# Optimization experiments

Hardware: AMD Instinct MI355X
Metric: run time of the kernel (lower is better)

## Reference

```python
import jax, jax.numpy as jnp
import numpy as np

R = 48          # n_comp (== n_comp_xy)
X = Y = Z = 300 # world_size
C = 27          # channels
N = 1_000_000   # query points
XYZ_MIN = 0.0
XYZ_MAX = 1.0


def _sample2d(plane, gh, gw):
    """Bilinear grid_sample, align_corners=True.
    plane: [R, H, W]; gh, gw: [N] normalized coords in [-1, 1] indexing H and W.
    Returns [N, R].
    """
    H, W = plane.shape[1], plane.shape[2]
    ih = (gh + 1.0) * 0.5 * (H - 1)
    iw = (gw + 1.0) * 0.5 * (W - 1)
    i0 = jnp.clip(jnp.floor(ih).astype(jnp.int32), 0, H - 1)
    j0 = jnp.clip(jnp.floor(iw).astype(jnp.int32), 0, W - 1)
    i1 = jnp.minimum(i0 + 1, H - 1)
    j1 = jnp.minimum(j0 + 1, W - 1)
    fh = (ih - i0.astype(ih.dtype))[:, None]  # [N,1]
    fw = (iw - j0.astype(iw.dtype))[:, None]
    p00 = plane[:, i0, j0].T  # [N,R]
    p01 = plane[:, i0, j1].T
    p10 = plane[:, i1, j0].T
    p11 = plane[:, i1, j1].T
    top = p00 * (1 - fw) + p01 * fw
    bot = p10 * (1 - fw) + p11 * fw
    return top * (1 - fh) + bot * fh


def _sample1d(vec, g):
    """Linear interp along length dim (width of the [*,*,L,1] torch vec is 1,
    sampled at 0 -> pure 1D interp).  vec: [R, L]; g: [N] in [-1,1] -> [N,R]."""
    L = vec.shape[1]
    ih = (g + 1.0) * 0.5 * (L - 1)
    i0 = jnp.clip(jnp.floor(ih).astype(jnp.int32), 0, L - 1)
    i1 = jnp.minimum(i0 + 1, L - 1)
    f = (ih - i0.astype(ih.dtype))[:, None]
    return vec[:, i0].T * (1 - f) + vec[:, i1].T * f


def setup_inputs() -> dict:
    key = jax.random.key(0)
    ks = jax.random.split(key, 8)
    return {
        "xyz": jax.random.uniform(ks[0], (N, 3), dtype=jnp.float32),
        "xy_plane": jax.random.normal(ks[1], (R, X, Y), dtype=jnp.float32) * 0.1,
        "xz_plane": jax.random.normal(ks[2], (R, X, Z), dtype=jnp.float32) * 0.1,
        "yz_plane": jax.random.normal(ks[3], (R, Y, Z), dtype=jnp.float32) * 0.1,
        "x_vec": jax.random.normal(ks[4], (R, X), dtype=jnp.float32) * 0.1,
        "y_vec": jax.random.normal(ks[5], (R, Y), dtype=jnp.float32) * 0.1,
        "z_vec": jax.random.normal(ks[6], (R, Z), dtype=jnp.float32) * 0.1,
        "f_vec": jax.random.uniform(ks[7], (3 * R, C), dtype=jnp.float32,
                                     minval=-0.1, maxval=0.1),
    }


def reference(xyz, xy_plane, xz_plane, yz_plane, x_vec, y_vec, z_vec, f_vec):
    # normalize to [-1, 1]
    g = (xyz - XYZ_MIN) / (XYZ_MAX - XYZ_MIN) * 2.0 - 1.0  # [N,3]
    gx, gy, gz = g[:, 0], g[:, 1], g[:, 2]
    xy_feat = _sample2d(xy_plane, gx, gy)  # [N,R]
    xz_feat = _sample2d(xz_plane, gx, gz)
    yz_feat = _sample2d(yz_plane, gy, gz)
    x_feat = _sample1d(x_vec, gx)
    y_feat = _sample1d(y_vec, gy)
    z_feat = _sample1d(z_vec, gz)
    feat = jnp.concatenate([xy_feat * z_feat, xz_feat * y_feat, yz_feat * x_feat],
                           axis=-1)  # [N, 3R]
    return feat @ f_vec  # [N, C]
```

## Files before the change

### kernel.cpp

```cpp
#include <hip/hip_runtime.h>

#define RR 48
#define GG 300
#define HW2 (GG * GG)
#define NPLANE (RR * HW2)
#define NVEC (RR * GG)
#define CC 27
#define NBUCK 32768
#define TP 64
#define TPP 65

struct Axis { int i0, i1; float f; };

__device__ __forceinline__ Axis axis_interp(float x) {
  float g = x * 2.0f - 1.0f;
  float ih = (g + 1.0f) * 0.5f * (float)(GG - 1);
  int i0 = (int)floorf(ih);
  i0 = i0 < 0 ? 0 : (i0 > GG - 1 ? GG - 1 : i0);
  int i1 = i0 + 1 > GG - 1 ? GG - 1 : i0 + 1;
  Axis a; a.i0 = i0; a.i1 = i1; a.f = ih - (float)i0;
  return a;
}

__device__ __forceinline__ unsigned part3(unsigned v) {
  unsigned r = 0;
  r |= (v & 1u);
  r |= (v & 2u) << 2;
  r |= (v & 4u) << 4;
  r |= (v & 8u) << 6;
  r |= (v & 16u) << 8;
  return r;
}

__device__ __forceinline__ int morton_key(float x, float y, float z) {
  int qx = (int)(x * 32.0f); qx = qx < 0 ? 0 : (qx > 31 ? 31 : qx);
  int qy = (int)(y * 32.0f); qy = qy < 0 ? 0 : (qy > 31 ? 31 : qy);
  int qz = (int)(z * 32.0f); qz = qz < 0 ? 0 : (qz > 31 ? 31 : qz);
  return (int)(part3((unsigned)qx) | (part3((unsigned)qy) << 1) | (part3((unsigned)qz) << 2));
}

__global__ void __launch_bounds__(256) hist_kernel(const float* __restrict__ xyz, int n,
                                                   int* __restrict__ offs) {
  int i = blockIdx.x * blockDim.x + threadIdx.x;
  if (i >= n) return;
  atomicAdd(&offs[morton_key(xyz[i * 3], xyz[i * 3 + 1], xyz[i * 3 + 2])], 1);
}

__global__ void __launch_bounds__(1024) scan_kernel(int* __restrict__ offs) {
  __shared__ int part[1024];
  int t = threadIdx.x;
  int base = t * (NBUCK / 1024);
  int loc[NBUCK / 1024];
  int s = 0;
#pragma unroll
  for (int i = 0; i < NBUCK / 1024; ++i) { loc[i] = offs[base + i]; s += loc[i]; }
  part[t] = s;
  __syncthreads();
  for (int off = 1; off < 1024; off <<= 1) {
    int u = (t >= off) ? part[t - off] : 0;
    __syncthreads();
    part[t] += u;
    __syncthreads();
  }
  int excl = (t == 0) ? 0 : part[t - 1];
#pragma unroll
  for (int i = 0; i < NBUCK / 1024; ++i) {
    int c = loc[i];
    offs[base + i] = excl;
    excl += c;
  }
}

__global__ void __launch_bounds__(256) scatter_kernel(const float* __restrict__ xyz, int n,
                                                      int* __restrict__ offs,
                                                      int* __restrict__ sidx,
                                                      float4* __restrict__ sxyz) {
  int i = blockIdx.x * blockDim.x + threadIdx.x;
  if (i >= n) return;
  float x = xyz[i * 3], y = xyz[i * 3 + 1], z = xyz[i * 3 + 2];
  int key = morton_key(x, y, z);
  int pos = atomicAdd(&offs[key], 1);
  if (sxyz) {
    sxyz[pos] = make_float4(x, y, z, __int_as_float(i));
  } else {
    sidx[pos] = i;
  }
}

__global__ void __launch_bounds__(256) transpose_planes(const float* __restrict__ p0,
                                                        const float* __restrict__ p1,
                                                        const float* __restrict__ p2,
                                                        float* __restrict__ t0,
                                                        float* __restrict__ t1,
                                                        float* __restrict__ t2) {
  __shared__ float tile[256 * 49];
  const float* in = (blockIdx.y == 0) ? p0 : (blockIdx.y == 1) ? p1 : p2;
  float* out = (blockIdx.y == 0) ? t0 : (blockIdx.y == 1) ? t1 : t2;
  int base = blockIdx.x * 256;
  int t = threadIdx.x;
  int pos = base + t;
#pragma unroll 1
  for (int r = 0; r < RR; ++r) {
    float v = (pos < HW2) ? in[r * HW2 + pos] : 0.f;
    tile[t * 49 + r] = v;
  }
  __syncthreads();
#pragma unroll 1
  for (int k = t; k < 256 * RR; k += 256) {
    int p = k / RR;
    int r = k - p * RR;
    int hw = base + p;
    if (hw < HW2) out[hw * RR + r] = tile[p * 49 + r];
  }
}

__global__ void __launch_bounds__(256) transpose_vecs(const float* __restrict__ v0,
                                                      const float* __restrict__ v1,
                                                      const float* __restrict__ v2,
                                                      float* __restrict__ t0,
                                                      float* __restrict__ t1,
                                                      float* __restrict__ t2) {
  int e = blockIdx.x * blockDim.x + threadIdx.x;
  if (e >= 3 * NVEC) return;
  int v = e / NVEC;
  int rem = e - v * NVEC;
  int i = rem / RR;
  int r = rem - i * RR;
  const float* in = (v == 0) ? v0 : (v == 1) ? v1 : v2;
  float* out = (v == 0) ? t0 : (v == 1) ? t1 : t2;
  out[i * RR + r] = in[r * GG + i];
}

__device__ __forceinline__ void gather_seg(const float* __restrict__ P, Axis ai, Axis aj,
                                           const float* __restrict__ V, Axis ak,
                                           int r4, float* __restrict__ dst) {
  float fi = ai.f, fj = aj.f, fk = ak.f;
  float w00 = (1.f - fi) * (1.f - fj);
  float w01 = (1.f - fi) * fj;
  float w10 = fi * (1.f - fj);
  float w11 = fi * fj;
  float omk = 1.f - fk;
  float4 q00 = *(const float4*)(P + (ai.i0 * GG + aj.i0) * RR + r4);
  float4 q01 = *(const float4*)(P + (ai.i0 * GG + aj.i1) * RR + r4);
  float4 q10 = *(const float4*)(P + (ai.i1 * GG + aj.i0) * RR + r4);
  float4 q11 = *(const float4*)(P + (ai.i1 * GG + aj.i1) * RR + r4);
  float4 b0 = *(const float4*)(V + ak.i0 * RR + r4);
  float4 b1 = *(const float4*)(V + ak.i1 * RR + r4);
  float t0 = (w00 * q00.x + w01 * q01.x + w10 * q10.x + w11 * q11.x) * (omk * b0.x + fk * b1.x);
  float t1 = (w00 * q00.y + w01 * q01.y + w10 * q10.y + w11 * q11.y) * (omk * b0.y + fk * b1.y);
  float t2 = (w00 * q00.z + w01 * q01.z + w10 * q10.z + w11 * q11.z) * (omk * b0.z + fk * b1.z);
  float t3 = (w00 * q00.w + w01 * q01.w + w10 * q10.w + w11 * q11.w) * (omk * b0.w + fk * b1.w);
  dst[(r4 + 0) * TPP] = t0;
  dst[(r4 + 1) * TPP] = t1;
  dst[(r4 + 2) * TPP] = t2;
  dst[(r4 + 3) * TPP] = t3;
}

__global__ void __launch_bounds__(256, 4) tensorf_fused(
    const float4* __restrict__ sxyz, const int* __restrict__ sidx,
    const float* __restrict__ xyz,
    const float* __restrict__ Txy, const float* __restrict__ Txz, const float* __restrict__ Tyz,
    const float* __restrict__ Tx, const float* __restrict__ Ty, const float* __restrict__ Tz,
    const float* __restrict__ F, float* __restrict__ out, int n, int chunkLen) {
  __shared__ float featT[144 * TPP];
  __shared__ int oiS[TP];
  int b = blockIdx.x;
  int nb = (b & 7) * chunkLen + (b >> 3);
  int base = nb * TP;
  int tid = threadIdx.x;
  int g = tid >> 4;
  int l = tid & 15;

#pragma unroll 1
  for (int it = 0; it < TP / 16; ++it) {
    int pl = (it << 4) + g;
    int sp = base + pl;
    if (sp < n) {
      float x, y, z;
      int oi;
      if (sxyz) {
        float4 p4 = sxyz[sp];
        x = p4.x; y = p4.y; z = p4.z;
        oi = __float_as_int(p4.w);
      } else {
        oi = sidx[sp];
        x = xyz[oi * 3 + 0];
        y = xyz[oi * 3 + 1];
        z = xyz[oi * 3 + 2];
      }
      if (l == 12) oiS[pl] = oi;
      Axis ax = axis_interp(x), ay = axis_interp(y), az = axis_interp(z);
      if (l < 12) {
        int r4 = l << 2;
        float* dst = &featT[pl];
        gather_seg(Txy, ax, ay, Tz, az, r4, dst + 0 * RR * TPP);
        gather_seg(Txz, ax, az, Ty, ay, r4, dst + 1 * RR * TPP);
        gather_seg(Tyz, ay, az, Tx, ax, r4, dst + 2 * RR * TPP);
      }
    }
  }
  __syncthreads();

  int p = tid & (TP - 1);
  int q = __builtin_amdgcn_readfirstlane(tid >> 6);
  int cbase = (q == 3) ? 20 : q * 7;
  const float* Fh = F + cbase;

  float acc[7];
#pragma unroll
  for (int c = 0; c < 7; ++c) acc[c] = 0.f;

#pragma unroll 4
  for (int k = 0; k < 144; ++k) {
    float fv = featT[k * TPP + p];
#pragma unroll
    for (int c = 0; c < 7; ++c) acc[c] = fmaf(fv, Fh[k * CC + c], acc[c]);
  }

  int sp = base + p;
  if (sp < n) {
    int oi = oiS[p];
    float* o = out + (size_t)oi * CC + cbase;
    if (q != 3) o[0] = acc[0];
#pragma unroll
    for (int c = 1; c < 7; ++c) o[c] = acc[c];
  }
}

__global__ void __launch_bounds__(256) tensorf_naive(
    const float* __restrict__ xyz,
    const float* __restrict__ Pxy, const float* __restrict__ Pxz, const float* __restrict__ Pyz,
    const float* __restrict__ Vx, const float* __restrict__ Vy, const float* __restrict__ Vz,
    const float* __restrict__ F, float* __restrict__ out, int n) {
  int idx = blockIdx.x * blockDim.x + threadIdx.x;
  if (idx >= n) return;
  float x = xyz[idx * 3], y = xyz[idx * 3 + 1], z = xyz[idx * 3 + 2];
  Axis ax = axis_interp(x), ay = axis_interp(y), az = axis_interp(z);
  float acc[CC];
#pragma unroll
  for (int c = 0; c < CC; ++c) acc[c] = 0.f;
  const float* Ps[3] = {Pxy, Pxz, Pyz};
  const float* Vs[3] = {Vz, Vy, Vx};
  Axis A[3][2] = {{ax, ay}, {ax, az}, {ay, az}};
  Axis K[3] = {az, ay, ax};
#pragma unroll 1
  for (int s = 0; s < 3; ++s) {
    Axis ai = A[s][0], aj = A[s][1], ak = K[s];
    float fi = ai.f, fj = aj.f, fk = ak.f;
    float w00 = (1.f - fi) * (1.f - fj), w01 = (1.f - fi) * fj;
    float w10 = fi * (1.f - fj), w11 = fi * fj, omk = 1.f - fk;
#pragma unroll 1
    for (int r = 0; r < RR; ++r) {
      const float* pr = Ps[s] + r * HW2;
      float ft = (w00 * pr[ai.i0 * GG + aj.i0] + w01 * pr[ai.i0 * GG + aj.i1] +
                  w10 * pr[ai.i1 * GG + aj.i0] + w11 * pr[ai.i1 * GG + aj.i1]) *
                 (omk * Vs[s][r * GG + ak.i0] + fk * Vs[s][r * GG + ak.i1]);
      const float* Fr = F + (s * RR + r) * CC;
#pragma unroll
      for (int c = 0; c < CC; ++c) acc[c] = fmaf(ft, Fr[c], acc[c]);
    }
  }
  float* o = out + (size_t)idx * CC;
#pragma unroll
  for (int c = 0; c < CC; ++c) o[c] = acc[c];
}

extern "C" void kernel_launch(void* const* d_in, const int* in_sizes, int n_in,
                              void* d_out, int out_size, void* d_ws, size_t ws_size,
                              hipStream_t stream) {
  const float* xyz = (const float*)d_in[0];
  const float* pxy = (const float*)d_in[1];
  const float* pxz = (const float*)d_in[2];
  const float* pyz = (const float*)d_in[3];
  const float* vx = (const float*)d_in[4];
  const float* vy = (const float*)d_in[5];
  const float* vz = (const float*)d_in[6];
  const float* F = (const float*)d_in[7];
  float* out = (float*)d_out;
  int n = in_sizes[0] / 3;
  int nblk = (n + 255) / 256;

  size_t fixed = (size_t)(3 * NPLANE + 3 * NVEC) * sizeof(float) +
                 (size_t)NBUCK * sizeof(int);
  size_t need1 = fixed + (size_t)n * sizeof(int);
  size_t need2 = fixed + (size_t)n * sizeof(float4);

  if (ws_size >= need1) {
    float* w = (float*)d_ws;
    float* Txy = w;
    float* Txz = Txy + NPLANE;
    float* Tyz = Txz + NPLANE;
    float* Tx = Tyz + NPLANE;
    float* Ty = Tx + NVEC;
    float* Tz = Ty + NVEC;
    int* offs = (int*)(Tz + NVEC);

    int* sidx = nullptr;
    float4* sxyz = nullptr;
    if (ws_size >= need2) sxyz = (float4*)(offs + NBUCK);
    else sidx = (int*)(offs + NBUCK);

    int tb = (HW2 + 255) / 256;
    dim3 tg(tb, 3);
    transpose_planes<<<tg, 256, 0, stream>>>(pxy, pxz, pyz, Txy, Txz, Tyz);
    int vb = (3 * NVEC + 255) / 256;
    transpose_vecs<<<vb, 256, 0, stream>>>(vx, vy, vz, Tx, Ty, Tz);

    hipMemsetAsync(offs, 0, (size_t)NBUCK * sizeof(int), stream);
    hist_kernel<<<nblk, 256, 0, stream>>>(xyz, n, offs);
    scan_kernel<<<1, 1024, 0, stream>>>(offs);
    scatter_kernel<<<nblk, 256, 0, stream>>>(xyz, n, offs, sidx, sxyz);

    int ntile = (n + TP - 1) / TP;
    int chunkLen = (ntile + 7) / 8;
    tensorf_fused<<<chunkLen * 8, 256, 0, stream>>>(sxyz, sidx, xyz, Txy, Txz, Tyz,
                                                    Tx, Ty, Tz, F, out, n, chunkLen);
  } else {
    tensorf_naive<<<nblk, 256, 0, stream>>>(xyz, pxy, pxz, pyz, vx, vy, vz, F, out, n);
  }
}
```

Before: 598.9 us.

## Fuse plane/vector transposes and histogram into one preprocess kernel with vectorized transpose

Merges the plane transpose, vector transpose and Morton histogram into a single launch, with block index ranges deciding which job each block does. This removes two kernel launches and lets the independent stages overlap. The plane transpose is reworked to use float4 global loads and stores through a row-major shared tile padded to 260 floats, in place of scalar strided accesses. The tile grows to about 50KB of shared memory, which may reduce occupancy for the histogram blocks that share the kernel.

```diff
diff --git a/kernel.cpp b/kernel.cpp
--- a/kernel.cpp
+++ b/kernel.cpp
@@ -10,6 +10,11 @@
 #define TP 64
 #define TPP 65
 
+#define PBLK ((HW2 + 255) / 256)
+#define PB3 (3 * PBLK)
+#define VBLK ((3 * NVEC + 255) / 256)
+#define TROW 260
+
 struct Axis { int i0, i1; float f; };
 
 __device__ __forceinline__ Axis axis_interp(float x) {
@@ -39,11 +44,76 @@
   return (int)(part3((unsigned)qx) | (part3((unsigned)qy) << 1) | (part3((unsigned)qz) << 2));
 }
 
-__global__ void __launch_bounds__(256) hist_kernel(const float* __restrict__ xyz, int n,
-                                                   int* __restrict__ offs) {
-  int i = blockIdx.x * blockDim.x + threadIdx.x;
-  if (i >= n) return;
-  atomicAdd(&offs[morton_key(xyz[i * 3], xyz[i * 3 + 1], xyz[i * 3 + 2])], 1);
+__global__ void __launch_bounds__(256) preprocess_kernel(
+    const float* __restrict__ p0, const float* __restrict__ p1, const float* __restrict__ p2,
+    float* __restrict__ t0, float* __restrict__ t1, float* __restrict__ t2,
+    const float* __restrict__ v0, const float* __restrict__ v1, const float* __restrict__ v2,
+    float* __restrict__ tv0, float* __restrict__ tv1, float* __restrict__ tv2,
+    const float* __restrict__ xyz, int n, int* __restrict__ offs) {
+  __shared__ float tile[RR * TROW];
+  int bb = blockIdx.x;
+  int t = threadIdx.x;
+
+  if (bb < PB3) {
+    int plane = bb / PBLK;
+    int chunk = bb - plane * PBLK;
+    const float* in = (plane == 0) ? p0 : (plane == 1) ? p1 : p2;
+    float* outp = (plane == 0) ? t0 : (plane == 1) ? t1 : t2;
+    int base = chunk * 256;
+    if (base + 256 <= HW2) {
+      int p4 = t & 63;
+      int rg = t >> 6;
+#pragma unroll 1
+      for (int i = 0; i < 12; ++i) {
+        int r = i * 4 + rg;
+        float4 v = *(const float4*)(in + (size_t)r * HW2 + base + p4 * 4);
+        *(float4*)&tile[r * TROW + p4 * 4] = v;
+      }
+      __syncthreads();
+#pragma unroll 1
+      for (int jj = 0; jj < 12; ++jj) {
+        int hw = ((jj & 3) << 6) + (t >> 2);
+        int c4 = ((jj >> 2) << 2) + (t & 3);
+        float4 w;
+        w.x = tile[(c4 * 4 + 0) * TROW + hw];
+        w.y = tile[(c4 * 4 + 1) * TROW + hw];
+        w.z = tile[(c4 * 4 + 2) * TROW + hw];
+        w.w = tile[(c4 * 4 + 3) * TROW + hw];
+        *(float4*)(outp + (size_t)(base + hw) * RR + c4 * 4) = w;
+      }
+    } else {
+      int pos = base + t;
+#pragma unroll 1
+      for (int r = 0; r < RR; ++r) {
+        float v = (pos < HW2) ? in[(size_t)r * HW2 + pos] : 0.f;
+        tile[r * TROW + t] = v;
+      }
+      __syncthreads();
+#pragma unroll 1
+      for (int k = t; k < 256 * RR; k += 256) {
+        int p = k / RR;
+        int r = k - p * RR;
+        int hw = base + p;
+        if (hw < HW2) outp[(size_t)hw * RR + r] = tile[r * TROW + p];
+      }
+    }
+  } else if (bb < PB3 + VBLK) {
+    int e = (bb - PB3) * 256 + t;
+    if (e < 3 * NVEC) {
+      int v = e / NVEC;
+      int rem = e - v * NVEC;
+      int i = rem / RR;
+      int r = rem - i * RR;
+      const float* in = (v == 0) ? v0 : (v == 1) ? v1 : v2;
+      float* out = (v == 0) ? tv0 : (v == 1) ? tv1 : tv2;
+      out[i * RR + r] = in[r * GG + i];
+    }
+  } else {
+    int i = (bb - PB3 - VBLK) * 256 + t;
+    if (i < n) {
+      atomicAdd(&offs[morton_key(xyz[i * 3], xyz[i * 3 + 1], xyz[i * 3 + 2])], 1);
+    }
+  }
 }
 
 __global__ void __launch_bounds__(1024) scan_kernel(int* __restrict__ offs) {
@@ -85,50 +155,6 @@
   } else {
     sidx[pos] = i;
   }
-}
-
-__global__ void __launch_bounds__(256) transpose_planes(const float* __restrict__ p0,
-                                                        const float* __restrict__ p1,
-                                                        const float* __restrict__ p2,
-                                                        float* __restrict__ t0,
-                                                        float* __restrict__ t1,
-                                                        float* __restrict__ t2) {
-  __shared__ float tile[256 * 49];
-  const float* in = (blockIdx.y == 0) ? p0 : (blockIdx.y == 1) ? p1 : p2;
-  float* out = (blockIdx.y == 0) ? t0 : (blockIdx.y == 1) ? t1 : t2;
-  int base = blockIdx.x * 256;
-  int t = threadIdx.x;
-  int pos = base + t;
-#pragma unroll 1
-  for (int r = 0; r < RR; ++r) {
-    float v = (pos < HW2) ? in[r * HW2 + pos] : 0.f;
-    tile[t * 49 + r] = v;
-  }
-  __syncthreads();
-#pragma unroll 1
-  for (int k = t; k < 256 * RR; k += 256) {
-    int p = k / RR;
-    int r = k - p * RR;
-    int hw = base + p;
-    if (hw < HW2) out[hw * RR + r] = tile[p * 49 + r];
-  }
-}
-
-__global__ void __launch_bounds__(256) transpose_vecs(const float* __restrict__ v0,
-                                                      const float* __restrict__ v1,
-                                                      const float* __restrict__ v2,
-                                                      float* __restrict__ t0,
-                                                      float* __restrict__ t1,
-                                                      float* __restrict__ t2) {
-  int e = blockIdx.x * blockDim.x + threadIdx.x;
-  if (e >= 3 * NVEC) return;
-  int v = e / NVEC;
-  int rem = e - v * NVEC;
-  int i = rem / RR;
-  int r = rem - i * RR;
-  const float* in = (v == 0) ? v0 : (v == 1) ? v1 : v2;
-  float* out = (v == 0) ? t0 : (v == 1) ? t1 : t2;
-  out[i * RR + r] = in[r * GG + i];
 }
 
 __device__ __forceinline__ void gather_seg(const float* __restrict__ P, Axis ai, Axis aj,
@@ -300,14 +326,9 @@
     if (ws_size >= need2) sxyz = (float4*)(offs + NBUCK);
     else sidx = (int*)(offs + NBUCK);
 
-    int tb = (HW2 + 255) / 256;
-    dim3 tg(tb, 3);
-    transpose_planes<<<tg, 256, 0, stream>>>(pxy, pxz, pyz, Txy, Txz, Tyz);
-    int vb = (3 * NVEC + 255) / 256;
-    transpose_vecs<<<vb, 256, 0, stream>>>(vx, vy, vz, Tx, Ty, Tz);
-
     hipMemsetAsync(offs, 0, (size_t)NBUCK * sizeof(int), stream);
-    hist_kernel<<<nblk, 256, 0, stream>>>(xyz, n, offs);
+    preprocess_kernel<<<PB3 + VBLK + nblk, 256, 0, stream>>>(
+        pxy, pxz, pyz, Txy, Txz, Tyz, vx, vy, vz, Tx, Ty, Tz, xyz, n, offs);
     scan_kernel<<<1, 1024, 0, stream>>>(offs);
     scatter_kernel<<<nblk, 256, 0, stream>>>(xyz, n, offs, sidx, sxyz);
 
```

Measured after the change: 538.7 us. 1.11x faster.
